# Kernel optimization log

Measured on AMD Instinct MI355X. Metric: run time of the kernel, lower is better.

The kernel has to match this reference:

```python
import jax, jax.numpy as jnp
import numpy as np

LEAK = 0.2

def leaky(x):
    return jnp.where(x > 0, x, LEAK * x)

def relu(x):
    return jnp.maximum(x, 0)

def conv1d(x, w):
    # x [B,Cin,L], w [Cout,Cin,3], stride 1, padding 1
    return jax.lax.conv_general_dilated(x, w, (1,), [(1, 1)],
        dimension_numbers=('NCH', 'OIH', 'NCH'))

def conv2d(x, w, pad, dil=1, groups=1):
    return jax.lax.conv_general_dilated(x, w, (1, 1), [(pad, pad), (pad, pad)],
        rhs_dilation=(dil, dil), feature_group_count=groups,
        dimension_numbers=('NCHW', 'OIHW', 'NCHW'))

def bn2d(x, p, eps=1e-5):
    # p: [4,C] = gamma, beta, running_mean, running_var (eval-mode BN)
    g, b, m, v = p
    s = (1, -1, 1, 1)
    return (x - m.reshape(s)) * (g.reshape(s) / jnp.sqrt(v.reshape(s) + eps)) + b.reshape(s)

def layernorm(x, g, b, eps=1e-5):
    mu = x.mean(-1, keepdims=True)
    var = ((x - mu) ** 2).mean(-1, keepdims=True)
    return (x - mu) / jnp.sqrt(var + eps) * g + b

def l2n(x, axis, eps):
    n = jnp.sqrt((x * x).sum(axis, keepdims=True))
    return x / jnp.maximum(n, eps)


def setup_inputs() -> dict:
    key = jax.random.key(0)
    B, C, H, W = 4, 64, 48, 48
    D, Fn, T, V = 256, 8, 4, 16
    E = 16  # orthogonal prototype embed dim
    ks = iter(jax.random.split(key, 64))
    def rn(shape, s=0.05):
        return jax.random.normal(next(ks), shape, jnp.float32) * s
    def bnp(c):
        return jnp.stack([1.0 + rn((c,), 0.1), rn((c,), 0.1), rn((c,), 0.1), 1.0 + jnp.abs(rn((c,), 0.1))])
    return dict(
        basis_vector_bank=jax.random.normal(next(ks), (T, V, D), jnp.float32),
        task_f=jax.random.normal(next(ks), (B, C, 16, 16), jnp.float32),
        img_f=jax.random.normal(next(ks), (B, C, H, W), jnp.float32),
        protos=jax.random.normal(next(ks), (T, E), jnp.float32),
        tA_w1=rn((E // 4, 1, 3)), tA_w2=rn((E // 2, E // 4, 3)),
        iA_w=rn((E // 2, C, 3, 3)), iA_bn=bnp(E // 2),
        at_w1=rn((E, Fn // 2 * E)), at_b1=rn((Fn // 2 * E,)),
        at_ln_g=jnp.ones((Fn // 2 * E,)), at_ln_b=jnp.zeros((Fn // 2 * E,)),
        at_w2=rn((Fn // 2 * E, Fn * E)), at_b2=rn((Fn * E,)),
        bv_t1=rn((D // 4, 1, 3)), bv_t2=rn((D // 2, D // 4, 3)),
        bv_ic1=rn((D // 4, C, 3, 3)), bv_bn1=bnp(D // 4),
        bv_ic2=rn((D // 2, D // 4, 3, 3)), bv_bn2=bnp(D // 2),
        bv_w1=rn((D, D // 4)), bv_b1=rn((D // 4,)),
        bv_ln_g=jnp.ones((D // 4,)), bv_ln_b=jnp.zeros((D // 4,)),
        bv_w2=rn((D // 4, D)), bv_b2=rn((D,)),
        m1_w1=rn((D, D // 4)), m1_b1=rn((D // 4,)),
        m1_ln_g=jnp.ones((D // 4,)), m1_ln_b=jnp.zeros((D // 4,)),
        m1_w2=rn((D // 4, C * C)), m1_b2=rn((C * C,)),
        m3_w1=rn((D, D // 4)), m3_b1=rn((D // 4,)),
        m3_ln_g=jnp.ones((D // 4,)), m3_ln_b=jnp.zeros((D // 4,)),
        m3_w2=rn((D // 4, 9 * C * C)), m3_b2=rn((9 * C * C,)),
        blr_bn=bnp(C),
        zc_w=rn((C, C, 1, 1), 0.01), zc_b=rn((C,), 0.01),
    )


def _forward(basis_vector_bank, task_f, img_f, protos, tA_w1, tA_w2, iA_w, iA_bn,
             at_w1, at_b1, at_ln_g, at_ln_b, at_w2, at_b2,
             bv_t1, bv_t2, bv_ic1, bv_bn1, bv_ic2, bv_bn2,
             bv_w1, bv_b1, bv_ln_g, bv_ln_b, bv_w2, bv_b2,
             m1_w1, m1_b1, m1_ln_g, m1_ln_b, m1_w2, m1_b2,
             m3_w1, m3_b1, m3_ln_g, m3_ln_b, m3_w2, m3_b2,
             blr_bn, zc_w, zc_b):
    T, V, D = basis_vector_bank.shape
    B, C, H, W = img_f.shape
    E = protos.shape[1]
    Fn = at_w2.shape[1] // E
    tau = 0.5

    # --- A2SI routing features ---
    xt = task_f.reshape(B, 1, -1)
    t1 = conv1d(leaky(conv1d(xt, tA_w1)), tA_w2).mean(-1)          # [B,E/2]
    i1 = leaky(bn2d(conv2d(img_f, iA_w, 1), iA_bn)).mean((2, 3))   # [B,E/2]
    f1 = jnp.concatenate([t1, i1], axis=1)                         # [B,E]
    h = relu(layernorm(f1 @ at_w1 + at_b1, at_ln_g, at_ln_b))
    tif = (h @ at_w2 + at_b2).reshape(B, E, Fn)                    # [B,E,F]
    logits = jnp.einsum('te,bef->bft', l2n(protos, -1, 1e-8), l2n(tif, 1, 1e-8))  # [B,F,T]

    # hard gumbel-softmax (straight-through), fixed noise key for determinism
    u = jax.random.uniform(jax.random.key(42), logits.shape, jnp.float32, 1e-10, 1.0)
    g = -jnp.log(-jnp.log(u))
    y = jax.nn.softmax((logits + g) / tau, axis=-1)
    idx = jnp.argmax(y, axis=-1)                                   # [B,F]
    y_hard = jax.nn.one_hot(idx, T, dtype=y.dtype)
    set_type = y_hard + y - jax.lax.stop_gradient(y)

    bank_flat = basis_vector_bank.reshape(T, V * D)
    sbvb = jnp.einsum('bft,tk->bfk', set_type, bank_flat).reshape(B, Fn, V, D)

    # --- BasisV_filter: filter feature ---
    xt2 = task_f.reshape(B, C, -1)
    rms = jnp.sqrt((xt2 ** 2).mean((1, 2), keepdims=True))
    xt2 = (xt2 / (rms + 1e-8)).reshape(B, 1, -1)
    te = conv1d(leaky(conv1d(xt2, bv_t1)), bv_t2).mean(-1)         # [B,D/2]
    ie = leaky(bn2d(conv2d(img_f, bv_ic1, 1), bv_bn1))
    ie = leaky(bn2d(conv2d(ie, bv_ic2, 1), bv_bn2)).mean((2, 3))   # [B,D/2]
    ff = jnp.concatenate([te, ie], axis=1)                         # [B,D]
    ff = relu(layernorm(ff @ bv_w1 + bv_b1, bv_ln_g, bv_ln_b)) @ bv_w2 + bv_b2

    # --- per-(batch,type) group gather/top-k/scatter, vectorized ---
    # group bank = bank of first filter with that type (hard one-hot -> type's bank)
    occ = idx[:, None, :] == jnp.arange(T)[None, :, None]          # [B,T,F]
    first = jnp.argmax(occ, axis=-1)                               # [B,T]
    Bg = jnp.take_along_axis(sbvb, first[:, :, None, None], axis=1)  # [B,T,V,D]
    # all rows of Q within a group are identical (filter_f expanded over F),
    # so S.max(0) == cosine(ff[b], Bg[b,t])
    scores = jnp.einsum('bd,btvd->btv', l2n(ff, -1, 1e-12), l2n(Bg, -1, 1e-12))
    order = jnp.argsort(-scores, axis=-1)                          # [B,T,V] topk order
    lt = jnp.tril(jnp.ones((Fn, Fn), bool), -1)                    # j < i
    rank = ((idx[:, :, None] == idx[:, None, :]) & lt).sum(-1)     # position in group
    bidx = jnp.arange(B)[:, None]
    sel = order[bidx, idx, rank]                                   # [B,F]
    bvf = Bg[bidx, idx, sel]                                       # [B,F,D]

    # --- per-filter dynamic convolutions ---
    w1 = relu(layernorm(bvf @ m1_w1 + m1_b1, m1_ln_g, m1_ln_b)) @ m1_w2 + m1_b2
    w1 = w1.reshape(B, Fn, C, C)                                   # [B,F,out,in]
    w3 = relu(layernorm(bvf @ m3_w1 + m3_b1, m3_ln_g, m3_ln_b)) @ m3_w2 + m3_b2
    w3 = w3.reshape(B * Fn, C, C, 3, 3)

    dp0 = jnp.einsum('bfoc,bchw->bfohw', w1, img_f)                # 1x1 branch
    xin = jnp.broadcast_to(img_f[:, None], (B, Fn, C, H, W)).reshape(1, B * Fn * C, H, W)
    ker = w3.reshape(B * Fn * C, C, 3, 3)
    dpd = [conv2d(xin, ker, d, dil=d, groups=B * Fn).reshape(B, Fn, C, H, W)
           for d in (1, 2, 3)]                                     # same-padded dilated 3x3
    t_ = idx[:, :, None, None, None]
    dp = jnp.where(t_ == 0, dp0, jnp.where(t_ == 1, dpd[0],
         jnp.where(t_ == 2, dpd[1], dpd[2])))                      # [B,F,C,H,W]

    x = leaky(bn2d(dp.reshape(B * Fn, C, H, W), blr_bn)).reshape(B, Fn, C, H, W).mean(1)
    a = conv2d(x, zc_w, 0) + zc_b.reshape(1, -1, 1, 1)
    return a + img_f


@jax.jit
def reference(basis_vector_bank, task_f, img_f, protos, tA_w1, tA_w2, iA_w, iA_bn,
              at_w1, at_b1, at_ln_g, at_ln_b, at_w2, at_b2,
              bv_t1, bv_t2, bv_ic1, bv_bn1, bv_ic2, bv_bn2,
              bv_w1, bv_b1, bv_ln_g, bv_ln_b, bv_w2, bv_b2,
              m1_w1, m1_b1, m1_ln_g, m1_ln_b, m1_w2, m1_b2,
              m3_w1, m3_b1, m3_ln_g, m3_ln_b, m3_w2, m3_b2,
              blr_bn, zc_w, zc_b):
    return _forward(basis_vector_bank, task_f, img_f, protos, tA_w1, tA_w2, iA_w, iA_bn,
                    at_w1, at_b1, at_ln_g, at_ln_b, at_w2, at_b2,
                    bv_t1, bv_t2, bv_ic1, bv_bn1, bv_ic2, bv_bn2,
                    bv_w1, bv_b1, bv_ln_g, bv_ln_b, bv_w2, bv_b2,
                    m1_w1, m1_b1, m1_ln_g, m1_ln_b, m1_w2, m1_b2,
                    m3_w1, m3_b1, m3_ln_g, m3_ln_b, m3_w2, m3_b2,
                    blr_bn, zc_w, zc_b)
```

## Files before the change

### kernel.cpp

```cpp
#include <hip/hip_runtime.h>
#include <math.h>

#define LEAKC 0.2f

#define NB 4
#define NC 64
#define LLEN 16384
#define HW 2304
#define PP 54
#define PHW 2916

typedef __attribute__((ext_vector_type(8))) short short8;
typedef __attribute__((ext_vector_type(4))) float floatx4;

__device__ __forceinline__ float leaky(float x){ return x > 0.f ? x : LEAKC*x; }

__device__ __forceinline__ float wave_sum64(float v){
  for(int off=32;off;off>>=1) v += __shfl_xor(v,off);
  return v;
}

__device__ __forceinline__ unsigned short f2bf(float x){
  unsigned u=__float_as_uint(x);
  unsigned r=u+0x7FFFu+((u>>16)&1u);
  return (unsigned short)(r>>16);
}

__device__ __forceinline__ void threefry2x32(unsigned k0, unsigned k1, unsigned& x0, unsigned& x1){
  unsigned ks0=k0, ks1=k1, ks2=k0^k1^0x1BD11BDAu;
  x0+=ks0; x1+=ks1;
  const int rot0[4]={13,15,26,6};
  const int rot1[4]={17,29,16,24};
#define TF_APPLY(rr) {for(int r=0;r<4;r++){x0+=x1; x1=(x1<<rr[r])|(x1>>(32-rr[r])); x1^=x0;}}
  TF_APPLY(rot0); x0+=ks1; x1+=ks2+1u;
  TF_APPLY(rot1); x0+=ks2; x1+=ks0+2u;
  TF_APPLY(rot0); x0+=ks0; x1+=ks1+3u;
  TF_APPLY(rot1); x0+=ks1; x1+=ks2+4u;
  TF_APPLY(rot0); x0+=ks2; x1+=ks0+5u;
#undef TF_APPLY
}

__device__ __forceinline__ float jax_uniform128(int i){
  unsigned x0=0u, x1=(unsigned)i;
  threefry2x32(0u,42u,x0,x1);
  unsigned bits = x0 ^ x1;
  unsigned fb=(bits>>9)|0x3f800000u;
  float f=__uint_as_float(fb)-1.0f;
  float u=f*(1.0f-1e-10f)+1e-10f;
  return fmaxf(1e-10f,u);
}

__global__ __launch_bounds__(256) void k_pre(const float* __restrict__ task_f,
                      const float* __restrict__ w1A, const float* __restrict__ w1B,
                      float* __restrict__ totA, float* __restrict__ a0A, float* __restrict__ aLA,
                      float* __restrict__ totB, float* __restrict__ a0B, float* __restrict__ aLB,
                      float* __restrict__ rmsacc,
                      const float* __restrict__ img,
                      const float* __restrict__ w1, const float* __restrict__ w2,
                      const float* __restrict__ wa,
                      unsigned short* __restrict__ imgTP,
                      unsigned short* __restrict__ W1T, unsigned short* __restrict__ W2T,
                      unsigned short* __restrict__ WAT){
  if(blockIdx.x<256){
    int b=blockIdx.x>>6, seg=blockIdx.x&63;
    const float* x=task_f+b*LLEN;
    float tA[4]={0,0,0,0};
    float tB[64];
#pragma unroll
    for(int c=0;c<64;c++) tB[c]=0.f;
    float sq=0.f;
    int l=seg*256+threadIdx.x;
    {
      float xm=(l>0)?x[l-1]:0.f;
      float xc=x[l];
      float xp=(l<LLEN-1)?x[l+1]:0.f;
      sq=xc*xc;
#pragma unroll
      for(int c=0;c<4;c++){
        float a=leaky(w1A[c*3+0]*xm + w1A[c*3+1]*xc + w1A[c*3+2]*xp);
        tA[c]=a;
        if(l==0) a0A[b*4+c]=a;
        if(l==LLEN-1) aLA[b*4+c]=a;
      }
#pragma unroll
      for(int c=0;c<64;c++){
        float a=leaky(w1B[c*3+0]*xm + w1B[c*3+1]*xc + w1B[c*3+2]*xp);
        tB[c]=a;
        if(l==0) a0B[b*64+c]=a;
        if(l==LLEN-1) aLB[b*64+c]=a;
      }
    }
    sq=wave_sum64(sq);
#pragma unroll
    for(int c=0;c<4;c++) tA[c]=wave_sum64(tA[c]);
#pragma unroll
    for(int c=0;c<64;c++){
      float v=tB[c];
      for(int off=32;off;off>>=1) v+=__shfl_down(v,off);
      tB[c]=v;
    }
    __shared__ float redB[4][64];
    __shared__ float redA[4][4];
    __shared__ float redQ[4];
    int wave=threadIdx.x>>6, lane=threadIdx.x&63;
    if(lane==0){
#pragma unroll
      for(int c=0;c<64;c++) redB[wave][c]=tB[c];
#pragma unroll
      for(int c=0;c<4;c++) redA[wave][c]=tA[c];
      redQ[wave]=sq;
    }
    __syncthreads();
    if(threadIdx.x<64){
      float s=redB[0][threadIdx.x]+redB[1][threadIdx.x]+redB[2][threadIdx.x]+redB[3][threadIdx.x];
      atomicAdd(&totB[b*64+threadIdx.x], s);
    } else if(threadIdx.x<68){
      int c=threadIdx.x-64;
      float s=redA[0][c]+redA[1][c]+redA[2][c]+redA[3][c];
      atomicAdd(&totA[b*4+c], s);
    } else if(threadIdx.x==68){
      atomicAdd(&rmsacc[b], redQ[0]+redQ[1]+redQ[2]+redQ[3]);
    }
  } else if(blockIdx.x<400){
    int blk=blockIdx.x-256;
    int b=blk/36, t=blk%36;
    int p0=t*64;
    __shared__ float tile[64][65];
    int pp=threadIdx.x&63, c4=threadIdx.x>>6;
    for(int r=0;r<16;r++){
      int c=c4*16+r;
      tile[c][pp]=img[(b*64+c)*HW + p0+pp];
    }
    __syncthreads();
    int pxl=threadIdx.x>>2, cg=(threadIdx.x&3)*16;
    unsigned out[8];
#pragma unroll
    for(int q=0;q<8;q++){
      unsigned lo=f2bf(tile[cg+2*q][pxl]);
      unsigned hi=f2bf(tile[cg+2*q+1][pxl]);
      out[q]=lo|(hi<<16);
    }
    int px=p0+pxl;
    int h=px/48, w=px-h*48;
    int poff=(h+3)*PP+(w+3);
    unsigned* dst=(unsigned*)(imgTP + ((size_t)(b*PHW+poff))*64 + cg);
#pragma unroll
    for(int q=0;q<8;q++) dst[q]=out[q];
  } else {
    int n=(blockIdx.x-400)*256+threadIdx.x;
    if(n<9*64*64){
      int tap=n>>12, oc=(n>>6)&63, c=n&63;
      W1T[n]=f2bf(w1[oc*576+c*9+tap]);
    } else if(n<9*64*64+9*128*64){
      int m=n-9*64*64;
      int tap=m/8192, r=m-tap*8192, oc=r>>6, c=r&63;
      W2T[m]=f2bf(w2[oc*576+c*9+tap]);
    } else {
      int q=n-9*64*64-9*128*64;
      if(q<9*16*64){
        int tap=q>>10, r=q&1023, o=r>>6, c=r&63;
        WAT[q]=(o<8)?f2bf(wa[o*576+c*9+tap]):(unsigned short)0;
      }
    }
  }
}

__global__ __launch_bounds__(256) void k_conv1(const unsigned short* __restrict__ imgTP,
                        const unsigned short* __restrict__ W1T,
                        const unsigned short* __restrict__ WAT,
                        const float* __restrict__ bn1, const float* __restrict__ bnA,
                        unsigned short* __restrict__ ie1TP, float* __restrict__ i1){
  int lane=threadIdx.x&63, mt=threadIdx.x>>6;
  int n0=lane&15, kg=lane>>4;
  if(blockIdx.x<96){
    int blk=blockIdx.x;
    int b=blk/24, hp=blk-b*24;
    int h0=hp*2;
    const unsigned short* ib=imgTP+(size_t)b*PHW*64;
    floatx4 acc[6];
#pragma unroll
    for(int i=0;i<6;i++) acc[i]=(floatx4){0.f,0.f,0.f,0.f};
#pragma unroll
    for(int ti=0;ti<3;ti++){
#pragma unroll
      for(int tj=0;tj<3;tj++){
        int tap=ti*3+tj;
        const unsigned short* Ab=W1T+(size_t)tap*4096;
#pragma unroll
        for(int c0=0;c0<64;c0+=32){
          short8 a=*(const short8*)(Ab+((mt*16+n0)*64+c0+kg*8));
#pragma unroll
          for(int rr=0;rr<2;rr++){
            int r=h0+rr+ti-1+3;
#pragma unroll
            for(int wc=0;wc<3;wc++){
              int w=wc*16+n0+tj-1+3;
              short8 bv=*(const short8*)(ib+((size_t)(r*PP+w)*64+c0+kg*8));
              acc[rr*3+wc]=__builtin_amdgcn_mfma_f32_16x16x32_bf16(a,bv,acc[rr*3+wc],0,0,0);
            }
          }
        }
      }
    }
    int obase=mt*16+kg*4;
    float scale[4],m_[4],be_[4];
#pragma unroll
    for(int reg=0;reg<4;reg++){
      int o=obase+reg;
      scale[reg]=bn1[o]/sqrtf(bn1[192+o]+1e-5f);
      m_[reg]=bn1[128+o]; be_[reg]=bn1[64+o];
    }
#pragma unroll
    for(int rr=0;rr<2;rr++){
#pragma unroll
      for(int wc=0;wc<3;wc++){
        int poff=(h0+rr+3)*PP + wc*16+n0+3;
        float v0=leaky((acc[rr*3+wc][0]-m_[0])*scale[0]+be_[0]);
        float v1=leaky((acc[rr*3+wc][1]-m_[1])*scale[1]+be_[1]);
        float v2=leaky((acc[rr*3+wc][2]-m_[2])*scale[2]+be_[2]);
        float v3=leaky((acc[rr*3+wc][3]-m_[3])*scale[3]+be_[3]);
        unsigned w0=f2bf(v0)|((unsigned)f2bf(v1)<<16);
        unsigned w1=f2bf(v2)|((unsigned)f2bf(v3)<<16);
        uint2 pk={w0,w1};
        *(uint2*)(ie1TP+((size_t)(b*PHW+poff)*64+obase))=pk;
      }
    }
  } else {
    int blk=blockIdx.x-96;
    int b=blk/6, hg=blk%6;
    int hp=hg*4+mt;
    int h0=hp*2;
    const unsigned short* ib=imgTP+(size_t)b*PHW*64;
    floatx4 acc[6];
#pragma unroll
    for(int i=0;i<6;i++) acc[i]=(floatx4){0.f,0.f,0.f,0.f};
#pragma unroll
    for(int ti=0;ti<3;ti++){
#pragma unroll
      for(int tj=0;tj<3;tj++){
        int tap=ti*3+tj;
        const unsigned short* Ab=WAT+(size_t)tap*1024;
#pragma unroll
        for(int c0=0;c0<64;c0+=32){
          short8 a=*(const short8*)(Ab+(n0*64+c0+kg*8));
#pragma unroll
          for(int rr=0;rr<2;rr++){
            int r=h0+rr+ti-1+3;
#pragma unroll
            for(int wc=0;wc<3;wc++){
              int w=wc*16+n0+tj-1+3;
              short8 bv=*(const short8*)(ib+((size_t)(r*PP+w)*64+c0+kg*8));
              acc[rr*3+wc]=__builtin_amdgcn_mfma_f32_16x16x32_bf16(a,bv,acc[rr*3+wc],0,0,0);
            }
          }
        }
      }
    }
    int obase=kg*4;
#pragma unroll
    for(int reg=0;reg<4;reg++){
      int o=obase+reg;
      float part=0;
      if(o<8){
        float scale=bnA[o]/sqrtf(bnA[24+o]+1e-5f);
        float m_=bnA[16+o], be_=bnA[8+o];
#pragma unroll
        for(int i=0;i<6;i++) part+=leaky((acc[i][reg]-m_)*scale+be_);
      }
      for(int off=1;off<16;off<<=1) part+=__shfl_xor(part,off);
      if(n0==0 && o<8) atomicAdd(&i1[b*8+o], part*(1.f/2304.f));
    }
  }
}

__global__ __launch_bounds__(256) void k_ic2M(const unsigned short* __restrict__ ie1TP,
                       const unsigned short* __restrict__ W2T,
                       const float* __restrict__ bn, float* __restrict__ ie){
  int blk=blockIdx.x;
  int b=blk/24, hp=blk-b*24;
  int mo=blockIdx.y*64;
  int lane=threadIdx.x&63, mt=threadIdx.x>>6;
  int n0=lane&15, kg=lane>>4;
  int h0=hp*2;
  const unsigned short* ib=ie1TP+(size_t)b*PHW*64;
  floatx4 acc[6];
#pragma unroll
  for(int i=0;i<6;i++) acc[i]=(floatx4){0.f,0.f,0.f,0.f};
#pragma unroll
  for(int ti=0;ti<3;ti++){
#pragma unroll
    for(int tj=0;tj<3;tj++){
      int tap=ti*3+tj;
      const unsigned short* Ab=W2T+(size_t)tap*8192;
#pragma unroll
      for(int c0=0;c0<64;c0+=32){
        short8 a=*(const short8*)(Ab+((mo+mt*16+n0)*64+c0+kg*8));
#pragma unroll
        for(int rr=0;rr<2;rr++){
          int r=h0+rr+ti-1+3;
#pragma unroll
          for(int wc=0;wc<3;wc++){
            int w=wc*16+n0+tj-1+3;
            short8 bv=*(const short8*)(ib+((size_t)(r*PP+w)*64+c0+kg*8));
            acc[rr*3+wc]=__builtin_amdgcn_mfma_f32_16x16x32_bf16(a,bv,acc[rr*3+wc],0,0,0);
          }
        }
      }
    }
  }
  int obase=mo+mt*16+kg*4;
#pragma unroll
  for(int reg=0;reg<4;reg++){
    int o=obase+reg;
    float scale=bn[o]/sqrtf(bn[384+o]+1e-5f);
    float m_=bn[256+o], be_=bn[128+o];
    float part=0;
#pragma unroll
    for(int i=0;i<6;i++) part+=leaky((acc[i][reg]-m_)*scale+be_);
    for(int off=1;off<16;off<<=1) part+=__shfl_xor(part,off);
    if(n0==0) atomicAdd(&ie[b*128+o], part*(1.f/2304.f));
  }
}

__global__ __launch_bounds__(256) void k_mid(
    const float* __restrict__ totA, const float* __restrict__ a0A, const float* __restrict__ aLA,
    const float* __restrict__ totB, const float* __restrict__ a0B, const float* __restrict__ aLB,
    const float* __restrict__ rmsacc,
    const float* __restrict__ tA_w2, const float* __restrict__ bv_t2,
    const float* __restrict__ i1, const float* __restrict__ ie,
    const float* __restrict__ at_w1, const float* __restrict__ at_b1,
    const float* __restrict__ at_ln_g, const float* __restrict__ at_ln_b,
    const float* __restrict__ at_w2, const float* __restrict__ at_b2,
    const float* __restrict__ protos,
    const float* __restrict__ bv_w1, const float* __restrict__ bv_b1,
    const float* __restrict__ bv_ln_g, const float* __restrict__ bv_ln_b,
    const float* __restrict__ bv_w2, const float* __restrict__ bv_b2,
    const float* __restrict__ bank,
    const float* __restrict__ m1_w1, const float* __restrict__ m1_b1,
    const float* __restrict__ m1_g,  const float* __restrict__ m1_bb,
    const float* __restrict__ m3_w1, const float* __restrict__ m3_b1,
    const float* __restrict__ m3_g,  const float* __restrict__ m3_bb,
    int* __restrict__ idxo, float* __restrict__ hid1, float* __restrict__ hid3){
  int b=blockIdx.x;
  int tid=threadIdx.x;
  int lane=tid&63, wv=tid>>6;
  const float invL=1.0f/16384.0f;
  __shared__ float sT[64], s0[64], sL[64];
  __shared__ float te_s[128], t1_s[8];
  __shared__ float f1[16], h[64], tif[128], tifn[128], tden[8], pden[4], pn[64], z[32];
  __shared__ int sidx[8], sfirst[4], srank[8], rows[8];
  __shared__ float fbuf[256], hh[64], ffn_s[256], finv_s;
  __shared__ float scores[64];
  __shared__ int order[64];
  __shared__ float bvf[2048];

  if(tid<64){ sT[tid]=totB[b*64+tid]; s0[tid]=a0B[b*64+tid]; sL[tid]=aLB[b*64+tid]; }
  __syncthreads();
  float scB=1.0f/(sqrtf(rmsacc[b]*invL)+1e-8f);
  if(tid<128){
    int c2=tid;
    const float* wr=bv_t2+c2*192;
    float s=0;
    for(int c1=0;c1<64;c1+=8){
      float4 q[6];
      const float4* r4=(const float4*)(wr+c1*3);
#pragma unroll
      for(int u=0;u<6;u++) q[u]=r4[u];
      const float* qq=(const float*)q;
#pragma unroll
      for(int u=0;u<8;u++){
        int c=c1+u;
        float T=sT[c], A0=s0[c], AL=sL[c];
        s += qq[u*3+0]*(T-AL) + qq[u*3+1]*T + qq[u*3+2]*(T-A0);
      }
    }
    te_s[c2]=s*invL*scB;
  } else if(tid<136){
    int c2=tid-128;
    float s=0;
    for(int c1=0;c1<4;c1++){
      float T=totA[b*4+c1], A0=a0A[b*4+c1], AL=aLA[b*4+c1];
      const float* w=&tA_w2[(c2*4+c1)*3];
      s += w[0]*(T-AL) + w[1]*T + w[2]*(T-A0);
    }
    t1_s[c2]=s*invL;
  }
  __syncthreads();

  if(tid<8) f1[tid]=t1_s[tid];
  else if(tid<16) f1[tid]=i1[b*8+tid-8];
  __syncthreads();
  if(tid<64){
    float s=at_b1[lane];
#pragma unroll
    for(int i=0;i<16;i++) s+=f1[i]*at_w1[i*64+lane];
    float mu=wave_sum64(s)*(1.f/64.f);
    float d=s-mu;
    float var=wave_sum64(d*d)*(1.f/64.f);
    h[lane]=fmaxf(d*(1.0f/sqrtf(var+1e-5f))*at_ln_g[lane]+at_ln_b[lane],0.f);
  }
  __syncthreads();
  if(tid<128){
    int n=tid;
    float a0=0,a1=0;
    for(int k=0;k<64;k+=2){
      a0+=h[k]*at_w2[k*128+n];
      a1+=h[k+1]*at_w2[(k+1)*128+n];
    }
    tif[n]=at_b2[n]+a0+a1;
  }
  __syncthreads();
  if(tid<8){
    int f=tid;
    float ss=0; for(int e=0;e<16;e++){float v=tif[e*8+f]; ss+=v*v;}
    tden[f]=fmaxf(sqrtf(ss),1e-8f);
  } else if(tid<12){
    int t=tid-8;
    float ss=0; for(int e=0;e<16;e++){float v=protos[t*16+e]; ss+=v*v;}
    pden[t]=fmaxf(sqrtf(ss),1e-8f);
  }
  __syncthreads();
  if(tid<128) tifn[tid]=tif[tid]/tden[tid&7];
  if(tid<64) pn[tid]=protos[tid]/pden[tid>>4];
  __syncthreads();
  if(tid<32){
    int f=tid>>2, t=tid&3;
    float ss=0;
#pragma unroll
    for(int e=0;e<16;e++) ss+=pn[t*16+e]*tifn[e*8+f];
    float u=jax_uniform128(b*32+f*4+t);
    float g=-logf(-logf(u));
    z[tid]=ss+g;
  }
  __syncthreads();
  if(tid<8){
    float best=z[tid*4]; int bi=0;
    for(int t=1;t<4;t++){ float v=z[tid*4+t]; if(v>best){best=v;bi=t;} }
    sidx[tid]=bi;
  }
  __syncthreads();
  if(tid<4){
    int t=tid;
    int fi=0;
    for(int f=7;f>=0;f--) if(sidx[f]==t) fi=f;
    sfirst[t]=fi;
  } else if(tid<12){
    int f=tid-4;
    int c=0; for(int f2=0;f2<f;f2++) if(sidx[f2]==sidx[f]) c++;
    srank[f]=c;
  }
  __syncthreads();

  if(tid<128) fbuf[tid]=te_s[tid];
  else fbuf[tid]=ie[b*128+tid-128];
  __syncthreads();
  if(tid<64){
    float a0=0,a1=0,a2=0,a3=0;
    for(int k=0;k<256;k+=4){
      a0+=fbuf[k]  *bv_w1[k*64+lane];
      a1+=fbuf[k+1]*bv_w1[(k+1)*64+lane];
      a2+=fbuf[k+2]*bv_w1[(k+2)*64+lane];
      a3+=fbuf[k+3]*bv_w1[(k+3)*64+lane];
    }
    float s=bv_b1[lane]+((a0+a1)+(a2+a3));
    float mu=wave_sum64(s)*(1.f/64.f);
    float d=s-mu;
    float var=wave_sum64(d*d)*(1.f/64.f);
    hh[lane]=fmaxf(d*(1.0f/sqrtf(var+1e-5f))*bv_ln_g[lane]+bv_ln_b[lane],0.f);
  }
  __syncthreads();
  {
    int n=tid;
    float a0=0,a1=0;
    for(int k=0;k<64;k+=2){
      a0+=hh[k]*bv_w2[k*256+n];
      a1+=hh[k+1]*bv_w2[(k+1)*256+n];
    }
    ffn_s[n]=bv_b2[n]+a0+a1;
  }
  __syncthreads();
  if(tid<64){
    float sq=0;
#pragma unroll
    for(int u=0;u<4;u++){ float v=ffn_s[u*64+lane]; sq+=v*v; }
    sq=wave_sum64(sq);
    if(lane==0) finv_s=1.0f/fmaxf(sqrtf(sq),1e-12f);
  }
  __syncthreads();
  ffn_s[tid]*=finv_s;
  __syncthreads();

  if(tid<64){
    int t=tid>>4, v=tid&15;
    int tt=sidx[sfirst[t]];
    const float4* row=(const float4*)(bank+(tt*16+v)*256);
    float sa=0,sb=0,na=0,nb=0;
    for(int d4=0;d4<64;d4+=2){
      float4 r1=row[d4], r2=row[d4+1];
      const float* f1p=&ffn_s[d4*4];
      sa+=f1p[0]*r1.x+f1p[1]*r1.y+f1p[2]*r1.z+f1p[3]*r1.w;
      na+=r1.x*r1.x+r1.y*r1.y+r1.z*r1.z+r1.w*r1.w;
      sb+=f1p[4]*r2.x+f1p[5]*r2.y+f1p[6]*r2.z+f1p[7]*r2.w;
      nb+=r2.x*r2.x+r2.y*r2.y+r2.z*r2.z+r2.w*r2.w;
    }
    scores[tid]=(sa+sb)/fmaxf(sqrtf(na+nb),1e-12f);
  }
  __syncthreads();
  if(tid<4){
    const float* sc=&scores[tid*16];
    unsigned used=0;
    for(int pk=0;pk<16;pk++){
      int best=-1; float bv=-1e30f;
      for(int v2=0;v2<16;v2++){
        if(used&(1u<<v2)) continue;
        float vv=sc[v2];
        if(best<0||vv>bv){bv=vv;best=v2;}
      }
      used|=1u<<best;
      order[tid*16+pk]=best;
    }
  }
  __syncthreads();
  if(tid<8){
    int t=sidx[tid];
    int v=order[t*16+srank[tid]];
    rows[tid]=t*16+v;
    idxo[b*8+tid]=t;
  }
  __syncthreads();

  for(int ii=tid;ii<2048;ii+=256){
    int r=ii>>8, d=ii&255;
    bvf[ii]=bank[rows[r]*256+d];
  }
  __syncthreads();
  for(int it=0;it<2;it++){
    int r=wv*2+it;
    const float* bp=&bvf[r*256];
    float a0=0,a1=0,a2=0,a3=0;
    float c0=0,c1=0,c2=0,c3=0;
    for(int d=0;d<256;d+=4){
      float b0=bp[d],b1=bp[d+1],b2=bp[d+2],b3=bp[d+3];
      a0+=b0*m1_w1[d*64+lane];
      a1+=b1*m1_w1[(d+1)*64+lane];
      a2+=b2*m1_w1[(d+2)*64+lane];
      a3+=b3*m1_w1[(d+3)*64+lane];
      c0+=b0*m3_w1[d*64+lane];
      c1+=b1*m3_w1[(d+1)*64+lane];
      c2+=b2*m3_w1[(d+2)*64+lane];
      c3+=b3*m3_w1[(d+3)*64+lane];
    }
    float s1=m1_b1[lane]+((a0+a1)+(a2+a3));
    float s3=m3_b1[lane]+((c0+c1)+(c2+c3));
    float mu=wave_sum64(s1)*(1.f/64.f);
    float dd=s1-mu;
    float var=wave_sum64(dd*dd)*(1.f/64.f);
    hid1[(b*8+r)*64+lane]=fmaxf(dd*(1.0f/sqrtf(var+1e-5f))*m1_g[lane]+m1_bb[lane],0.f);
    mu=wave_sum64(s3)*(1.f/64.f);
    dd=s3-mu;
    var=wave_sum64(dd*dd)*(1.f/64.f);
    hid3[(b*8+r)*64+lane]=fmaxf(dd*(1.0f/sqrtf(var+1e-5f))*m3_g[lane]+m3_bb[lane],0.f);
  }
}

__global__ __launch_bounds__(256) void k_heads(const float* __restrict__ hid1, const float* __restrict__ hid3,
                        const float* __restrict__ w2a, const float* __restrict__ b2a,
                        const float* __restrict__ w2b, const float* __restrict__ b2b,
                        unsigned short* __restrict__ A1, unsigned short* __restrict__ A3){
  __shared__ float hl[2048];
  if(blockIdx.x<16){
    int n=blockIdx.x*256+threadIdx.x;
    for(int i=threadIdx.x;i<2048;i+=256) hl[i]=hid1[i];
    __syncthreads();
    float wcol[64];
#pragma unroll
    for(int k=0;k<64;k++) wcol[k]=w2a[k*4096+n];
    float bb=b2a[n];
    for(int bf=0;bf<32;bf++){
      float s=bb;
#pragma unroll
      for(int k=0;k<64;k++) s+=hl[bf*64+k]*wcol[k];
      A1[bf*4096+n]=f2bf(s);
    }
  } else {
    int n=(blockIdx.x-16)*256+threadIdx.x;
    for(int i=threadIdx.x;i<2048;i+=256) hl[i]=hid3[i];
    __syncthreads();
    float wcol[64];
#pragma unroll
    for(int k=0;k<64;k++) wcol[k]=w2b[(size_t)k*36864+n];
    float bb=b2b[n];
    int o=n/576, rem=n-o*576;
    int c=rem/9, tap=rem-c*9;
    size_t base=((size_t)tap*64+o)*64+c;
    for(int bf=0;bf<32;bf++){
      float s=bb;
#pragma unroll
      for(int k=0;k<64;k++) s+=hl[bf*64+k]*wcol[k];
      A3[(size_t)bf*9*4096+base]=f2bf(s);
    }
  }
}

#define SLABP 72
__global__ __launch_bounds__(512) void k_dynF(const unsigned short* __restrict__ imgTP,
                       const unsigned short* __restrict__ A1, const unsigned short* __restrict__ A3,
                       const int* __restrict__ idx, const float* __restrict__ bn,
                       const float* __restrict__ zc_w, const float* __restrict__ zc_b,
                       const float* __restrict__ img, float* __restrict__ out){
  int blk=blockIdx.x;
  int b=blk/48, r0=blk-b*48;
  int tid=threadIdx.x;
  int lane=tid&63, w8=tid>>6;
  int mt=w8&3, fh=w8>>2;
  int n0=lane&15, kg=lane>>4;
  __shared__ unsigned short slab[7*54*SLABP];
  __shared__ float xl[64*50];
  __shared__ float zl[4096];
  for(int i=tid;i<4096;i+=512) zl[i]=zc_w[i];
  for(int i=tid;i<3200;i+=512) xl[i]=0.f;
  {
    const unsigned short* ibase=imgTP+((size_t)b*PHW+(size_t)r0*PP)*64;
    for(int e=tid;e<7*54*8;e+=512){
      int rr=e/(54*8), rem=e-rr*54*8, w=rem>>3, ck=rem&7;
      uint4 v=*(const uint4*)(ibase + ((size_t)(rr*PP+w))*64 + ck*8);
      *(uint4*)(slab + (rr*54+w)*SLABP + ck*8)=v;
    }
  }
  __syncthreads();
  int obase=mt*16+kg*4;
  float scale[4],m_[4],be_[4];
#pragma unroll
  for(int reg=0;reg<4;reg++){
    int o=obase+reg;
    scale[reg]=bn[o]/sqrtf(bn[192+o]+1e-5f);
    m_[reg]=bn[128+o]; be_[reg]=bn[64+o];
  }
  float xsum[3][4];
#pragma unroll
  for(int wc=0;wc<3;wc++)
#pragma unroll
    for(int reg=0;reg<4;reg++) xsum[wc][reg]=0.f;
  for(int f=fh*4;f<fh*4+4;f++){
    int bf=b*8+f;
    int tt=idx[bf];
    floatx4 acc[3];
#pragma unroll
    for(int i=0;i<3;i++) acc[i]=(floatx4){0.f,0.f,0.f,0.f};
    if(tt==0){
      const unsigned short* Ab=A1+(size_t)bf*4096;
#pragma unroll
      for(int c0=0;c0<64;c0+=32){
        short8 a=*(const short8*)(Ab+((mt*16+n0)*64+c0+kg*8));
#pragma unroll
        for(int wc=0;wc<3;wc++){
          short8 bv=*(const short8*)(slab + (3*54 + wc*16+n0+3)*SLABP + c0+kg*8);
          acc[wc]=__builtin_amdgcn_mfma_f32_16x16x32_bf16(a,bv,acc[wc],0,0,0);
        }
      }
    } else {
      int d=tt;
      const unsigned short* A3b=A3+(size_t)bf*9*4096;
#pragma unroll
      for(int ti=0;ti<3;ti++){
        int lr=d*(ti-1)+3;
#pragma unroll
        for(int tj=0;tj<3;tj++){
          int tap=ti*3+tj;
          int dw=d*(tj-1)+3;
          const unsigned short* Ab=A3b+(size_t)tap*4096;
#pragma unroll
          for(int c0=0;c0<64;c0+=32){
            short8 a=*(const short8*)(Ab+((mt*16+n0)*64+c0+kg*8));
#pragma unroll
            for(int wc=0;wc<3;wc++){
              short8 bv=*(const short8*)(slab + (lr*54 + wc*16+n0+dw)*SLABP + c0+kg*8);
              acc[wc]=__builtin_amdgcn_mfma_f32_16x16x32_bf16(a,bv,acc[wc],0,0,0);
            }
          }
        }
      }
    }
#pragma unroll
    for(int wc=0;wc<3;wc++)
#pragma unroll
      for(int reg=0;reg<4;reg++)
        xsum[wc][reg]+=leaky((acc[wc][reg]-m_[reg])*scale[reg]+be_[reg]);
  }
#pragma unroll
  for(int wc=0;wc<3;wc++)
#pragma unroll
    for(int reg=0;reg<4;reg++)
      atomicAdd(&xl[(obase+reg)*50 + wc*16+n0], xsum[wc][reg]*0.125f);
  __syncthreads();
  size_t base=(size_t)b*64*HW + r0*48;
  for(int e=tid;e<3072;e+=512){
    int o=e/48, px=e-o*48;
    float s=zc_b[o];
#pragma unroll
    for(int c=0;c<64;c++) s+=zl[o*64+c]*xl[c*50+px];
    size_t a=base+(size_t)o*HW+px;
    out[a]=s+img[a];
  }
}

extern "C" void kernel_launch(void* const* d_in, const int* in_sizes, int n_in,
                              void* d_out, int out_size, void* d_ws, size_t ws_size,
                              hipStream_t stream){
  const float* bank   =(const float*)d_in[0];
  const float* task_f =(const float*)d_in[1];
  const float* img_f  =(const float*)d_in[2];
  const float* protos =(const float*)d_in[3];
  const float* tA_w1  =(const float*)d_in[4];
  const float* tA_w2  =(const float*)d_in[5];
  const float* iA_w   =(const float*)d_in[6];
  const float* iA_bn  =(const float*)d_in[7];
  const float* at_w1  =(const float*)d_in[8];
  const float* at_b1  =(const float*)d_in[9];
  const float* at_ln_g=(const float*)d_in[10];
  const float* at_ln_b=(const float*)d_in[11];
  const float* at_w2  =(const float*)d_in[12];
  const float* at_b2  =(const float*)d_in[13];
  const float* bv_t1  =(const float*)d_in[14];
  const float* bv_t2  =(const float*)d_in[15];
  const float* bv_ic1 =(const float*)d_in[16];
  const float* bv_bn1 =(const float*)d_in[17];
  const float* bv_ic2 =(const float*)d_in[18];
  const float* bv_bn2 =(const float*)d_in[19];
  const float* bv_w1  =(const float*)d_in[20];
  const float* bv_b1  =(const float*)d_in[21];
  const float* bv_ln_g=(const float*)d_in[22];
  const float* bv_ln_b=(const float*)d_in[23];
  const float* bv_w2  =(const float*)d_in[24];
  const float* bv_b2  =(const float*)d_in[25];
  const float* m1_w1  =(const float*)d_in[26];
  const float* m1_b1  =(const float*)d_in[27];
  const float* m1_ln_g=(const float*)d_in[28];
  const float* m1_ln_b=(const float*)d_in[29];
  const float* m1_w2  =(const float*)d_in[30];
  const float* m1_b2  =(const float*)d_in[31];
  const float* m3_w1  =(const float*)d_in[32];
  const float* m3_b1  =(const float*)d_in[33];
  const float* m3_ln_g=(const float*)d_in[34];
  const float* m3_ln_b=(const float*)d_in[35];
  const float* m3_w2  =(const float*)d_in[36];
  const float* m3_b2  =(const float*)d_in[37];
  const float* blr_bn =(const float*)d_in[38];
  const float* zc_w   =(const float*)d_in[39];
  const float* zc_b   =(const float*)d_in[40];

  float* ws=(float*)d_ws;
  float* totA=ws+0;       float* a0A=ws+16;      float* aLA=ws+32;
  float* totB=ws+48;      float* a0B=ws+304;     float* aLB=ws+560;
  float* rmsacc=ws+816;   float* i1 =ws+820;     float* ie =ws+852;
  int*   idxp  =(int*)(ws+2932);
  float* hid1=ws+3044;    float* hid3=ws+5092;
  unsigned short* A1p  =(unsigned short*)(ws+7140);
  unsigned short* A3p  =(unsigned short*)(ws+72676);
  unsigned short* imgTP=(unsigned short*)(ws+662500);
  unsigned short* ie1TP=(unsigned short*)(ws+1035748);
  unsigned short* W1Tp =(unsigned short*)(ws+1408996);
  unsigned short* W2Tp =(unsigned short*)(ws+1427428);
  unsigned short* WATp =(unsigned short*)(ws+1464292);

  hipMemsetAsync(ws, 0, 1364*sizeof(float), stream);
  hipMemsetAsync(imgTP, 0, 2*746496*sizeof(unsigned short), stream);

  k_pre<<<868,256,0,stream>>>(task_f, tA_w1, bv_t1,
                              totA, a0A, aLA, totB, a0B, aLB, rmsacc,
                              img_f, bv_ic1, bv_ic2, iA_w, imgTP, W1Tp, W2Tp, WATp);
  k_conv1<<<120,256,0,stream>>>(imgTP, W1Tp, WATp, bv_bn1, iA_bn, ie1TP, i1);
  k_ic2M<<<dim3(96,2),256,0,stream>>>(ie1TP, W2Tp, bv_bn2, ie);
  k_mid<<<4,256,0,stream>>>(totA,a0A,aLA,totB,a0B,aLB, rmsacc, tA_w2, bv_t2, i1, ie,
                            at_w1, at_b1, at_ln_g, at_ln_b, at_w2, at_b2, protos,
                            bv_w1, bv_b1, bv_ln_g, bv_ln_b, bv_w2, bv_b2, bank,
                            m1_w1, m1_b1, m1_ln_g, m1_ln_b,
                            m3_w1, m3_b1, m3_ln_g, m3_ln_b,
                            idxp, hid1, hid3);
  k_heads<<<160,256,0,stream>>>(hid1, hid3, m1_w2, m1_b2, m3_w2, m3_b2, A1p, A3p);
  k_dynF<<<192,512,0,stream>>>(imgTP, A1p, A3p, idxp, blr_bn, zc_w, zc_b, img_f, (float*)d_out);

  (void)in_sizes; (void)n_in; (void)out_size; (void)ws_size;
}
```

Baseline: 292.0 us.

## Widen k_mid to 512 threads with split-K partial sums and prewarm weights into L2

k_mid runs on only 4 blocks and is latency bound. Its block size doubles to 512 threads and each small matvec (bv_t2, at_w2, bv_w1, bv_w2, prototype scores, head matvecs) is split across more threads, with partial sums reduced through shared memory. k_pre also gets 16 extra blocks that touch one element in every 64 bytes of the weights k_mid reads later, so those lines are already in L2/cache when k_mid runs. This adds extra barriers and a few extra k_pre blocks, and the warm loads may be evicted before k_mid runs.

```diff
diff --git a/kernel.cpp b/kernel.cpp
--- a/kernel.cpp
+++ b/kernel.cpp
@@ -60,7 +60,11 @@
                       const float* __restrict__ wa,
                       unsigned short* __restrict__ imgTP,
                       unsigned short* __restrict__ W1T, unsigned short* __restrict__ W2T,
-                      unsigned short* __restrict__ WAT){
+                      unsigned short* __restrict__ WAT,
+                      const float* __restrict__ mw1, const float* __restrict__ mw3,
+                      const float* __restrict__ bvw1p, const float* __restrict__ bvw2p,
+                      const float* __restrict__ bvt2p, const float* __restrict__ atw2p,
+                      const float* __restrict__ bankp, float* __restrict__ warm){
   if(blockIdx.x<256){
     int b=blockIdx.x>>6, seg=blockIdx.x&63;
     const float* x=task_f+b*LLEN;
@@ -146,7 +150,7 @@
     unsigned* dst=(unsigned*)(imgTP + ((size_t)(b*PHW+poff))*64 + cg);
 #pragma unroll
     for(int q=0;q<8;q++) dst[q]=out[q];
-  } else {
+  } else if(blockIdx.x<868){
     int n=(blockIdx.x-400)*256+threadIdx.x;
     if(n<9*64*64){
       int tap=n>>12, oc=(n>>6)&63, c=n&63;
@@ -162,6 +166,17 @@
         WAT[q]=(o<8)?f2bf(wa[o*576+c*9+tap]):(unsigned short)0;
       }
     }
+  } else {
+    int t=(blockIdx.x-868)*256+threadIdx.x;
+    float a=0.f;
+    for(int i=t;i*16<16384;i+=4096) a+=mw1[i*16];
+    for(int i=t;i*16<16384;i+=4096) a+=mw3[i*16];
+    for(int i=t;i*16<16384;i+=4096) a+=bvw1p[i*16];
+    for(int i=t;i*16<16384;i+=4096) a+=bvw2p[i*16];
+    for(int i=t;i*16<24576;i+=4096) a+=bvt2p[i*16];
+    for(int i=t;i*16<8192;i+=4096) a+=atw2p[i*16];
+    for(int i=t;i*16<16384;i+=4096) a+=bankp[i*16];
+    warm[t&1023]=a;
   }
 }
 
@@ -322,7 +337,7 @@
   }
 }
 
-__global__ __launch_bounds__(256) void k_mid(
+__global__ __launch_bounds__(512,1) void k_mid(
     const float* __restrict__ totA, const float* __restrict__ a0A, const float* __restrict__ aLA,
     const float* __restrict__ totB, const float* __restrict__ a0B, const float* __restrict__ aLB,
     const float* __restrict__ rmsacc,
@@ -346,6 +361,7 @@
   int lane=tid&63, wv=tid>>6;
   const float invL=1.0f/16384.0f;
   __shared__ float sT[64], s0[64], sL[64];
+  __shared__ float part[512];
   __shared__ float te_s[128], t1_s[8];
   __shared__ float f1[16], h[64], tif[128], tifn[128], tden[8], pden[4], pn[64], z[32];
   __shared__ int sidx[8], sfirst[4], srank[8], rows[8];
@@ -357,11 +373,11 @@
   if(tid<64){ sT[tid]=totB[b*64+tid]; s0[tid]=a0B[b*64+tid]; sL[tid]=aLB[b*64+tid]; }
   __syncthreads();
   float scB=1.0f/(sqrtf(rmsacc[b]*invL)+1e-8f);
-  if(tid<128){
-    int c2=tid;
+  if(tid<256){
+    int c2=tid&127, h2=tid>>7;
     const float* wr=bv_t2+c2*192;
     float s=0;
-    for(int c1=0;c1<64;c1+=8){
+    for(int c1=h2*32;c1<h2*32+32;c1+=8){
       float4 q[6];
       const float4* r4=(const float4*)(wr+c1*3);
 #pragma unroll
@@ -374,9 +390,9 @@
         s += qq[u*3+0]*(T-AL) + qq[u*3+1]*T + qq[u*3+2]*(T-A0);
       }
     }
-    te_s[c2]=s*invL*scB;
-  } else if(tid<136){
-    int c2=tid-128;
+    part[tid]=s;
+  } else if(tid>=384 && tid<392){
+    int c2=tid-384;
     float s=0;
     for(int c1=0;c1<4;c1++){
       float T=totA[b*4+c1], A0=a0A[b*4+c1], AL=aLA[b*4+c1];
@@ -386,6 +402,8 @@
     t1_s[c2]=s*invL;
   }
   __syncthreads();
+  if(tid<128) te_s[tid]=(part[tid]+part[tid+128])*invL*scB;
+  __syncthreads();
 
   if(tid<8) f1[tid]=t1_s[tid];
   else if(tid<16) f1[tid]=i1[b*8+tid-8];
@@ -400,15 +418,17 @@
     h[lane]=fmaxf(d*(1.0f/sqrtf(var+1e-5f))*at_ln_g[lane]+at_ln_b[lane],0.f);
   }
   __syncthreads();
-  if(tid<128){
-    int n=tid;
+  if(tid<256){
+    int n=tid&127, h2=tid>>7;
     float a0=0,a1=0;
-    for(int k=0;k<64;k+=2){
+    for(int k=h2*32;k<h2*32+32;k+=2){
       a0+=h[k]*at_w2[k*128+n];
       a1+=h[k+1]*at_w2[(k+1)*128+n];
     }
-    tif[n]=at_b2[n]+a0+a1;
-  }
+    part[tid]=a0+a1;
+  }
+  __syncthreads();
+  if(tid<128) tif[tid]=at_b2[tid]+part[tid]+part[tid+128];
   __syncthreads();
   if(tid<8){
     int f=tid;
@@ -452,17 +472,22 @@
   __syncthreads();
 
   if(tid<128) fbuf[tid]=te_s[tid];
-  else fbuf[tid]=ie[b*128+tid-128];
+  else if(tid<256) fbuf[tid]=ie[b*128+tid-128];
+  __syncthreads();
+  if(tid<256){
+    int l64=tid&63, q=tid>>6;
+    float a0=0,a1=0,a2=0,a3=0;
+    for(int k=q*64;k<q*64+64;k+=4){
+      a0+=fbuf[k]  *bv_w1[k*64+l64];
+      a1+=fbuf[k+1]*bv_w1[(k+1)*64+l64];
+      a2+=fbuf[k+2]*bv_w1[(k+2)*64+l64];
+      a3+=fbuf[k+3]*bv_w1[(k+3)*64+l64];
+    }
+    part[tid]=((a0+a1)+(a2+a3));
+  }
   __syncthreads();
   if(tid<64){
-    float a0=0,a1=0,a2=0,a3=0;
-    for(int k=0;k<256;k+=4){
-      a0+=fbuf[k]  *bv_w1[k*64+lane];
-      a1+=fbuf[k+1]*bv_w1[(k+1)*64+lane];
-      a2+=fbuf[k+2]*bv_w1[(k+2)*64+lane];
-      a3+=fbuf[k+3]*bv_w1[(k+3)*64+lane];
-    }
-    float s=bv_b1[lane]+((a0+a1)+(a2+a3));
+    float s=bv_b1[lane]+part[lane]+part[64+lane]+part[128+lane]+part[192+lane];
     float mu=wave_sum64(s)*(1.f/64.f);
     float d=s-mu;
     float var=wave_sum64(d*d)*(1.f/64.f);
@@ -470,14 +495,16 @@
   }
   __syncthreads();
   {
-    int n=tid;
+    int n=tid&255, h2=tid>>8;
     float a0=0,a1=0;
-    for(int k=0;k<64;k+=2){
+    for(int k=h2*32;k<h2*32+32;k+=2){
       a0+=hh[k]*bv_w2[k*256+n];
       a1+=hh[k+1]*bv_w2[(k+1)*256+n];
     }
-    ffn_s[n]=bv_b2[n]+a0+a1;
-  }
+    part[tid]=a0+a1;
+  }
+  __syncthreads();
+  if(tid<256) ffn_s[tid]=bv_b2[tid]+part[tid]+part[tid+256];
   __syncthreads();
   if(tid<64){
     float sq=0;
@@ -487,24 +514,26 @@
     if(lane==0) finv_s=1.0f/fmaxf(sqrtf(sq),1e-12f);
   }
   __syncthreads();
-  ffn_s[tid]*=finv_s;
-  __syncthreads();
-
-  if(tid<64){
-    int t=tid>>4, v=tid&15;
+  if(tid<256) ffn_s[tid]*=finv_s;
+  __syncthreads();
+
+  if(tid<128){
+    int it=tid&63, h2=tid>>6;
+    int t=it>>4, v=it&15;
     int tt=sidx[sfirst[t]];
     const float4* row=(const float4*)(bank+(tt*16+v)*256);
-    float sa=0,sb=0,na=0,nb=0;
-    for(int d4=0;d4<64;d4+=2){
-      float4 r1=row[d4], r2=row[d4+1];
-      const float* f1p=&ffn_s[d4*4];
-      sa+=f1p[0]*r1.x+f1p[1]*r1.y+f1p[2]*r1.z+f1p[3]*r1.w;
-      na+=r1.x*r1.x+r1.y*r1.y+r1.z*r1.z+r1.w*r1.w;
-      sb+=f1p[4]*r2.x+f1p[5]*r2.y+f1p[6]*r2.z+f1p[7]*r2.w;
-      nb+=r2.x*r2.x+r2.y*r2.y+r2.z*r2.z+r2.w*r2.w;
-    }
-    scores[tid]=(sa+sb)/fmaxf(sqrtf(na+nb),1e-12f);
-  }
+    float sa=0,na=0;
+    for(int d4=h2*32;d4<h2*32+32;d4++){
+      float4 r=row[d4];
+      const float* fp=&ffn_s[d4*4];
+      sa+=fp[0]*r.x+fp[1]*r.y+fp[2]*r.z+fp[3]*r.w;
+      na+=r.x*r.x+r.y*r.y+r.z*r.z+r.w*r.w;
+    }
+    part[tid]=sa;
+    part[256+tid]=na;
+  }
+  __syncthreads();
+  if(tid<64) scores[tid]=(part[tid]+part[tid+64])/fmaxf(sqrtf(part[256+tid]+part[320+tid]),1e-12f);
   __syncthreads();
   if(tid<4){
     const float* sc=&scores[tid*16];
@@ -529,13 +558,13 @@
   }
   __syncthreads();
 
-  for(int ii=tid;ii<2048;ii+=256){
+  for(int ii=tid;ii<2048;ii+=512){
     int r=ii>>8, d=ii&255;
     bvf[ii]=bank[rows[r]*256+d];
   }
   __syncthreads();
-  for(int it=0;it<2;it++){
-    int r=wv*2+it;
+  {
+    int r=wv;
     const float* bp=&bvf[r*256];
     float a0=0,a1=0,a2=0,a3=0;
     float c0=0,c1=0,c2=0,c3=0;
@@ -762,16 +791,18 @@
   unsigned short* W1Tp =(unsigned short*)(ws+1408996);
   unsigned short* W2Tp =(unsigned short*)(ws+1427428);
   unsigned short* WATp =(unsigned short*)(ws+1464292);
+  float* warm =ws+1468900;
 
   hipMemsetAsync(ws, 0, 1364*sizeof(float), stream);
   hipMemsetAsync(imgTP, 0, 2*746496*sizeof(unsigned short), stream);
 
-  k_pre<<<868,256,0,stream>>>(task_f, tA_w1, bv_t1,
+  k_pre<<<884,256,0,stream>>>(task_f, tA_w1, bv_t1,
                               totA, a0A, aLA, totB, a0B, aLB, rmsacc,
-                              img_f, bv_ic1, bv_ic2, iA_w, imgTP, W1Tp, W2Tp, WATp);
+                              img_f, bv_ic1, bv_ic2, iA_w, imgTP, W1Tp, W2Tp, WATp,
+                              m1_w1, m3_w1, bv_w1, bv_w2, bv_t2, at_w2, bank, warm);
   k_conv1<<<120,256,0,stream>>>(imgTP, W1Tp, WATp, bv_bn1, iA_bn, ie1TP, i1);
   k_ic2M<<<dim3(96,2),256,0,stream>>>(ie1TP, W2Tp, bv_bn2, ie);
-  k_mid<<<4,256,0,stream>>>(totA,a0A,aLA,totB,a0B,aLB, rmsacc, tA_w2, bv_t2, i1, ie,
+  k_mid<<<4,512,0,stream>>>(totA,a0A,aLA,totB,a0B,aLB, rmsacc, tA_w2, bv_t2, i1, ie,
                             at_w1, at_b1, at_ln_g, at_ln_b, at_w2, at_b2, protos,
                             bv_w1, bv_b1, bv_ln_g, bv_ln_b, bv_w2, bv_b2, bank,
                             m1_w1, m1_b1, m1_ln_g, m1_ln_b,
```

Result: no change. 287.0 us (-1.7%).
